# Kernel tuning notes

Measured on AMD Instinct MI355X. Metric: run time of the kernel, lower is better.

Reference implementation:

```python
import jax, jax.numpy as jnp
import numpy as np
import math

H, W = 1024, 1024

def setup_inputs() -> dict:
    key = jax.random.key(0)
    img = jax.random.uniform(key, (H, W), dtype=jnp.float32) * 255.0
    return {"InputImage": img}

def _phase_congruency(img):
    nrows, ncols = img.shape
    minWaveLength, mult = 3.0, 2.1
    nscale, norient = 5, 6
    sigmaOnf, k, cutOff, g = 0.55, 2.0, 0.5, 10.0
    eps = 1e-4

    cy, cx = nrows // 2, ncols // 2
    yy, xx = jnp.mgrid[0:nrows, 0:ncols]
    yy = (yy - cy) / nrows
    xx = (xx - cx) / ncols
    radius = jnp.sqrt(xx ** 2 + yy ** 2)
    radius = radius.at[cy, cx].set(1.0)
    theta = jnp.arctan2(-yy, xx)
    sintheta, costheta = jnp.sin(theta), jnp.cos(theta)

    # low-pass Butterworth (order 15, cutoff 0.45)
    normradius = radius / (jnp.abs(xx).max() * 2)
    lowpass = 1.0 / (1.0 + (normradius / 0.45) ** 30)

    # log-Gabor radial filters, [nscale, H, W]
    s = jnp.arange(nscale, dtype=jnp.float32)
    fo = 1.0 / (minWaveLength * mult ** s)            # [S]
    logGabor = jnp.exp(-jnp.log(radius[None] * (1.0 / fo)[:, None, None]) ** 2
                       / (2 * math.log(sigmaOnf) ** 2))
    annular = logGabor * lowpass[None]
    annular = annular.at[:, cy, cx].set(0.0)

    # angular spread, [norient, H, W]
    angl = jnp.arange(norient, dtype=jnp.float32) * (math.pi / norient)
    cosA, sinA = jnp.cos(angl), jnp.sin(angl)
    ds = sintheta[None] * cosA[:, None, None] - costheta[None] * sinA[:, None, None]
    dc = costheta[None] * cosA[:, None, None] + sintheta[None] * sinA[:, None, None]
    dtheta = jnp.minimum(jnp.abs(jnp.arctan2(ds, dc)) * (norient / 2), math.pi)
    spread = (jnp.cos(dtheta) + 1.0) / 2.0

    # full filter bank [O, S, H, W], shifted to DFT layout
    filt = jnp.fft.ifftshift(spread[:, None] * annular[None], axes=(-2, -1))

    F = jnp.fft.fft2(img)                              # complex64
    # cv2.idft is unscaled -> multiply numpy-style ifft by N
    z = jnp.fft.ifft2(filt * F[None, None]) * (nrows * ncols)   # [O,S,H,W]
    # original code: E (even) = channel 1 = Im(z), O (odd) = channel 0 = Re(z)
    E, O = z.imag, z.real
    An = jnp.abs(z)

    sumE = E.sum(axis=1)        # [O,H,W]
    sumO = O.sum(axis=1)
    sumAn = An.sum(axis=1)
    maxAn = An.max(axis=1)
    tau = jnp.median(An[:, 0].reshape(norient, -1), axis=1) / math.sqrt(math.log(4.0))

    XEnergy = jnp.sqrt(sumE ** 2 + sumO ** 2) + eps
    MeanE = sumE / XEnergy
    MeanO = sumO / XEnergy
    Energy = (E * MeanE[:, None] + O * MeanO[:, None]
              - jnp.abs(E * MeanO[:, None] - O * MeanE[:, None])).sum(axis=1)

    totalTau = tau * (1 - (1 / mult) ** nscale) / (1 - 1 / mult)   # [O]
    T = totalTau * math.sqrt(math.pi / 2) + k * totalTau * math.sqrt((4 - math.pi) / 2)
    Energy = jnp.maximum(Energy - T[:, None, None], 0.0)

    width = (sumAn / (maxAn + eps) - 1.0) / (nscale - 1)
    weight = 1.0 / (1.0 + jnp.exp((cutOff - width) * g))
    PC = weight * Energy / sumAn                       # [O,H,W]

    covx = PC * cosA[:, None, None]
    covy = PC * sinA[:, None, None]
    covx2 = (covx ** 2).sum(axis=0) / (norient / 2)
    covy2 = (covy ** 2).sum(axis=0) / (norient / 2)
    covxy = 4.0 * (covx * covy).sum(axis=0) / norient
    denom = jnp.sqrt(covxy ** 2 + (covx2 - covy2) ** 2) + eps
    M = (covy2 + covx2 + denom) / 2.0
    m = (covy2 + covx2 - denom) / 2.0
    return M, m

def reference(InputImage):
    M, m = _phase_congruency(InputImage)
    return (M, m)
```

## Files before the change

### kernel.cpp

```cpp
#include <hip/hip_runtime.h>
#include <math.h>

typedef float2 c2;

#define S_IDX(i) ((i) ^ (((i) >> 5) & 15))

__device__ __forceinline__ c2 cmul(c2 a, c2 b){
  return make_float2(a.x*b.x - a.y*b.y, a.x*b.y + a.y*b.x);
}

__constant__ float c_foinv[5] = {3.0f, 6.3f, 13.23f, 27.783f, 58.3443f};
__constant__ float c_lnfo[5]  = {1.0986123f, 1.8405496f, 2.5824700f, 3.3244106f, 4.0663219f};
__constant__ float c_angl[6]  = {0.0f, 0.5235988f, 1.0471976f, 1.5707963f, 2.0943951f, 2.6179939f};
__constant__ float c_cosA[6] = {1.0f, 0.8660254038f, 0.5f, 6.123233996e-17f, -0.5f, -0.8660254038f};
__constant__ float c_sinA[6] = {0.0f, 0.5f, 0.8660254038f, 1.0f, 0.8660254038f, 0.5f};

template<int SIGN>
__device__ __forceinline__ void make_tw(int t, c2* w){
#pragma unroll
  for (int k = 0; k < 5; ++k){
    const int s = 1 << (2*k);
    const float ang = (float)SIGN * 0.00613592315154256f * (float)(t & ~(s-1));
    sincosf(ang, &w[k].y, &w[k].x);
  }
}

template<int SIGN>
__device__ __forceinline__ void fft1024(c2* bufA, c2* bufB, int t, const c2* w){
  c2* cur = bufA; c2* oth = bufB;
#pragma unroll
  for (int k = 0; k < 5; ++k){
    const int s = 1 << (2*k);
    const int q = t & (s - 1);
    c2 a = cur[S_IDX(t)];
    c2 b = cur[S_IDX(t + 256)];
    c2 c = cur[S_IDX(t + 512)];
    c2 d = cur[S_IDX(t + 768)];
    c2 w1 = w[k];
    c2 w2 = cmul(w1, w1);
    c2 w3 = cmul(w2, w1);
    c2 apc = make_float2(a.x + c.x, a.y + c.y);
    c2 amc = make_float2(a.x - c.x, a.y - c.y);
    c2 bpd = make_float2(b.x + d.x, b.y + d.y);
    c2 bmd = make_float2(b.x - d.x, b.y - d.y);
    c2 y0 = make_float2(apc.x + bpd.x, apc.y + bpd.y);
    c2 e2 = make_float2(apc.x - bpd.x, apc.y - bpd.y);
    const float S4 = (float)SIGN;
    c2 u1 = make_float2(amc.x - S4*bmd.y, amc.y + S4*bmd.x);
    c2 u3 = make_float2(amc.x + S4*bmd.y, amc.y - S4*bmd.x);
    c2 y1 = cmul(u1, w1);
    c2 y2 = cmul(e2, w2);
    c2 y3 = cmul(u3, w3);
    const int bw = 4*t - 3*q;
    oth[S_IDX(bw)]       = y0;
    oth[S_IDX(bw + s)]   = y1;
    oth[S_IDX(bw + 2*s)] = y2;
    oth[S_IDX(bw + 3*s)] = y3;
    c2* tmp = cur; cur = oth; oth = tmp;
    __syncthreads();
  }
}

__device__ __forceinline__ float filt_eval(int q, int a, float xx,
                                           float cosA, float sinA, float foinv){
  const float yy = (float)(q < 512 ? q : q - 1024) * (1.0f/1024.0f);
  const float r2 = xx*xx + yy*yy;
  const bool isdc = (q == 0) && (a == 0);
  const float radius = isdc ? 1.0f : sqrtf(r2);
  const float tt = radius * (1.0f/0.45f);
  const float t2 = tt*tt, t4 = t2*t2, t8 = t4*t4, t16 = t8*t8;
  const float lp = 1.0f / (1.0f + t16*t8*t4*t2);
  const float lnr = logf(radius * foinv);
  const float lg = expf(-lnr*lnr * 1.3989572f);
  const float ir = 1.0f / radius;
  const float st = -yy * ir, ct = xx * ir;
  const float dsv = st*cosA - ct*sinA;
  const float dcv = ct*cosA + st*sinA;
  const float dth = fminf(fabsf(atan2f(dsv, dcv)) * 3.0f, 3.14159274f);
  const float spr = 0.5f * (cosf(dth) + 1.0f);
  const float f = lg * lp * spr;
  return isdc ? 0.0f : f;
}

__global__ __launch_bounds__(256) void k_filt_tab(float* __restrict__ lnrT, float* __restrict__ thetaT){
  const int a = blockIdx.x;
  const int t = threadIdx.x;
  const float xx = (float)(a < 512 ? a : a - 1024) * (1.0f/1024.0f);
#pragma unroll
  for (int j = 0; j < 4; ++j){
    const int q = t + 256*j;
    const float yy = (float)(q < 512 ? q : q - 1024) * (1.0f/1024.0f);
    const float radius = sqrtf(xx*xx + yy*yy);
    float lnr = logf(radius);
    if (a == 0 && q == 0) lnr = __int_as_float(0x7F800000);
    const float th = atan2f(-yy, xx);
    lnrT[a*1024 + q] = lnr;
    thetaT[a*1024 + q] = th;
  }
}

__global__ __launch_bounds__(256) void k_fft_fwd_real(const float* __restrict__ in, c2* __restrict__ out){
  const int t = threadIdx.x;
  __shared__ c2 bufA[1024];
  __shared__ c2 bufB[1024];
  c2 w[5]; make_tw<-1>(t, w);
  for (int rr = 0; rr < 4; ++rr){
    const int row = blockIdx.x * 4 + rr;
    const float* src = in + (size_t)row * 1024;
    c2* dst = out + (size_t)row * 1024;
#pragma unroll
    for (int j = 0; j < 4; ++j){
      const int q = t + 256*j;
      bufA[S_IDX(q)] = make_float2(src[q], 0.0f);
    }
    __syncthreads();
    fft1024<-1>(bufA, bufB, t, w);
#pragma unroll
    for (int j = 0; j < 4; ++j){ const int q = t + 256*j; dst[q] = bufB[S_IDX(q)]; }
    __syncthreads();
  }
}

__global__ __launch_bounds__(256) void k_fft_fwd_ip(c2* __restrict__ Z){
  const int t = threadIdx.x;
  c2* base = Z + (size_t)blockIdx.y * 1048576;
  __shared__ c2 bufA[1024];
  __shared__ c2 bufB[1024];
  c2 w[5]; make_tw<-1>(t, w);
  for (int rr = 0; rr < 4; ++rr){
    const int row = blockIdx.x * 4 + rr;
    c2* p = base + (size_t)row * 1024;
#pragma unroll
    for (int j = 0; j < 4; ++j){ const int q = t + 256*j; bufA[S_IDX(q)] = p[q]; }
    __syncthreads();
    fft1024<-1>(bufA, bufB, t, w);
#pragma unroll
    for (int j = 0; j < 4; ++j){ const int q = t + 256*j; p[q] = bufB[S_IDX(q)]; }
    __syncthreads();
  }
}

__global__ __launch_bounds__(256) void k_fft_inv_filter_t(const c2* __restrict__ F, c2* __restrict__ Z,
                                                          const float* __restrict__ lnrT,
                                                          const float* __restrict__ thetaT){
  const int t = threadIdx.x;
  const int gslot = blockIdx.y;
  const int orient = gslot / 5;
  const int scale = gslot - orient*5;
  const float lnfo = c_lnfo[scale];
  const float angl = c_angl[orient];
  __shared__ c2 bufA[1024];
  __shared__ c2 bufB[1024];
  c2 w[5]; make_tw<1>(t, w);
  for (int rr = 0; rr < 4; ++rr){
    const int row = blockIdx.x * 4 + rr;
    const c2* src = F + (size_t)row * 1024;
    const float* lnrR = lnrT + (size_t)row * 1024;
    const float* thR  = thetaT + (size_t)row * 1024;
    c2* dst = Z + (size_t)gslot * 1048576 + (size_t)row * 1024;
#pragma unroll
    for (int j = 0; j < 4; ++j){
      const int q = t + 256*j;
      const c2 v = src[q];
      const float lnr = lnrR[q];
      const float th  = thR[q];
      const float u = lnr + lnfo;
      const float lg = __expf(-u*u * 1.3989572f);
      const float lp = 1.0f / (1.0f + __expf(fmaf(30.0f, lnr, 23.955231f)));
      float d = th - angl;
      if (d <= -3.14159274f) d += 6.28318548f;
      const float dth = fminf(fabsf(d) * 3.0f, 3.14159274f);
      const float spr = 0.5f * (__cosf(dth) + 1.0f);
      const float f = lg * lp * spr;
      bufA[S_IDX(q)] = make_float2(v.x*f, v.y*f);
    }
    __syncthreads();
    fft1024<1>(bufA, bufB, t, w);
#pragma unroll
    for (int j = 0; j < 4; ++j){ const int q = t + 256*j; dst[q] = bufB[S_IDX(q)]; }
    __syncthreads();
  }
}

__global__ __launch_bounds__(256) void k_fft_inv_filter_b(const c2* __restrict__ F, c2* __restrict__ Z,
                                                          int slot0){
  const int t = threadIdx.x;
  const int gslot = slot0 + blockIdx.y;
  const int orient = gslot / 5;
  const int scale = gslot - orient*5;
  const float foinv = c_foinv[scale];
  const float cosA = c_cosA[orient], sinA = c_sinA[orient];
  __shared__ c2 bufA[1024];
  __shared__ c2 bufB[1024];
  c2 w[5]; make_tw<1>(t, w);
  for (int rr = 0; rr < 4; ++rr){
    const int row = blockIdx.x * 4 + rr;
    const c2* src = F + (size_t)row * 1024;
    c2* dst = Z + (size_t)blockIdx.y * 1048576 + (size_t)row * 1024;
    const float xx = (float)(row < 512 ? row : row - 1024) * (1.0f/1024.0f);
#pragma unroll
    for (int j = 0; j < 4; ++j){
      const int q = t + 256*j;
      const c2 v = src[q];
      const float f = filt_eval(q, row, xx, cosA, sinA, foinv);
      bufA[S_IDX(q)] = make_float2(v.x*f, v.y*f);
    }
    __syncthreads();
    fft1024<1>(bufA, bufB, t, w);
#pragma unroll
    for (int j = 0; j < 4; ++j){ const int q = t + 256*j; dst[q] = bufB[S_IDX(q)]; }
    __syncthreads();
  }
}

__global__ __launch_bounds__(256) void k_fft_inv_ip(c2* __restrict__ Z){
  const int t = threadIdx.x;
  c2* base = Z + (size_t)blockIdx.y * 1048576;
  __shared__ c2 bufA[1024];
  __shared__ c2 bufB[1024];
  c2 w[5]; make_tw<1>(t, w);
  for (int rr = 0; rr < 4; ++rr){
    const int row = blockIdx.x * 4 + rr;
    c2* p = base + (size_t)row * 1024;
#pragma unroll
    for (int j = 0; j < 4; ++j){ const int q = t + 256*j; bufA[S_IDX(q)] = p[q]; }
    __syncthreads();
    fft1024<1>(bufA, bufB, t, w);
#pragma unroll
    for (int j = 0; j < 4; ++j){ const int q = t + 256*j; p[q] = bufB[S_IDX(q)]; }
    __syncthreads();
  }
}

__global__ void k_transpose_ip(c2* __restrict__ Zb){
  __shared__ c2 A[32][33];
  __shared__ c2 B[32][33];
  c2* base = Zb + (size_t)blockIdx.y * 1048576;
  const int p = blockIdx.x;
  int i = (int)floorf((sqrtf(8.0f*(float)p + 1.0f) - 1.0f) * 0.5f);
  while ((i+1)*(i+2)/2 <= p) ++i;
  while (i*(i+1)/2 > p) --i;
  const int j = p - i*(i+1)/2;
  const int tx = threadIdx.x, ty = threadIdx.y;
  const int r0 = i*32, c0 = j*32;
#pragma unroll
  for (int jj = 0; jj < 32; jj += 8)
    A[ty+jj][tx] = base[(size_t)(r0+ty+jj)*1024 + c0+tx];
  if (i != j){
#pragma unroll
    for (int jj = 0; jj < 32; jj += 8)
      B[ty+jj][tx] = base[(size_t)(c0+ty+jj)*1024 + r0+tx];
  }
  __syncthreads();
#pragma unroll
  for (int jj = 0; jj < 32; jj += 8)
    base[(size_t)(c0+ty+jj)*1024 + r0+tx] = A[tx][ty+jj];
  if (i != j){
#pragma unroll
    for (int jj = 0; jj < 32; jj += 8)
      base[(size_t)(r0+ty+jj)*1024 + c0+tx] = B[tx][ty+jj];
  }
}


__device__ __forceinline__ unsigned amp_bits(const c2 v){
  return __float_as_uint(sqrtf(v.x*v.x + v.y*v.y));
}

__global__ __launch_bounds__(256) void k_med_p1b(const c2* __restrict__ Zb, size_t oStride,
                                                 unsigned* __restrict__ g1, int oBase){
  __shared__ unsigned h[4][4096];
  const int t = threadIdx.x;
  const int wv = t >> 6;
  const c2* z0 = Zb + (size_t)blockIdx.y * oStride;
  unsigned* gg = g1 + (size_t)(oBase + blockIdx.y) * 4096;
  for (int j = t; j < 4*4096; j += 256) ((unsigned*)h)[j] = 0;
  __syncthreads();
  const int base = blockIdx.x * 16384;
  for (int it = 0; it < 64; ++it){
    const unsigned bits = amp_bits(z0[base + it*256 + t]);
    atomicAdd(&h[wv][bits >> 20], 1u);
  }
  __syncthreads();
  for (int j = t; j < 4096; j += 256){
    const unsigned s = h[0][j] + h[1][j] + h[2][j] + h[3][j];
    if (s) atomicAdd(&gg[j], s);
  }
}

__global__ __launch_bounds__(256) void k_sel1b(const unsigned* __restrict__ g1,
                                               unsigned* __restrict__ sc1,
                                               unsigned* __restrict__ g2, int oBase){
  __shared__ unsigned partial[256];
  const int t = threadIdx.x;
  const int oo = oBase + blockIdx.x;
  const unsigned* gg = g1 + (size_t)oo * 4096;
  unsigned loc[16]; unsigned s = 0;
#pragma unroll
  for (int j = 0; j < 16; ++j){ loc[j] = gg[t*16 + j]; s += loc[j]; }
  partial[t] = s;
  __syncthreads();
  unsigned p = 0;
  for (int u = 0; u < t; ++u) p += partial[u];
  for (int which = 0; which < 2; ++which){
    const unsigned R = 524287u + (unsigned)which;
    if (R >= p && R - p < s){
      unsigned cum = p;
      for (int j = 0; j < 16; ++j){
        if (R - cum < loc[j]){ sc1[oo*4 + which*2] = (unsigned)(t*16 + j); sc1[oo*4 + which*2+1] = R - cum; break; }
        cum += loc[j];
      }
    }
  }
  for (int j = t; j < 8192; j += 256) g2[(size_t)oo*8192 + j] = 0;
}

__global__ __launch_bounds__(256) void k_med_p2b(const c2* __restrict__ Zb, size_t oStride,
                                                 const unsigned* __restrict__ sc1,
                                                 unsigned* __restrict__ g2, int oBase){
  __shared__ unsigned h[2][4096];
  const int t = threadIdx.x;
  const int oo = oBase + blockIdx.y;
  const c2* z0 = Zb + (size_t)blockIdx.y * oStride;
  unsigned* gg = g2 + (size_t)oo * 8192;
  for (int j = t; j < 8192; j += 256) ((unsigned*)h)[j] = 0;
  __syncthreads();
  const unsigned b0 = sc1[oo*4 + 0], b1 = sc1[oo*4 + 2];
  const int base = blockIdx.x * 16384;
  for (int it = 0; it < 64; ++it){
    const unsigned bits = amp_bits(z0[base + it*256 + t]);
    const unsigned top = bits >> 20;
    const unsigned mid = (bits >> 8) & 4095u;
    if (top == b0)      atomicAdd(&h[0][mid], 1u);
    else if (top == b1) atomicAdd(&h[1][mid], 1u);
  }
  __syncthreads();
  for (int j = t; j < 4096; j += 256){
    if (h[0][j]) atomicAdd(&gg[j], h[0][j]);
    if (h[1][j]) atomicAdd(&gg[4096 + j], h[1][j]);
  }
}

__global__ __launch_bounds__(256) void k_sel2b(const unsigned* __restrict__ g2,
                                               const unsigned* __restrict__ sc1,
                                               unsigned* __restrict__ sc2,
                                               unsigned* __restrict__ g3, int oBase){
  __shared__ unsigned partial[256];
  const int t = threadIdx.x;
  const int oo = oBase + blockIdx.x;
  const unsigned b0 = sc1[oo*4+0], lr0 = sc1[oo*4+1], b1 = sc1[oo*4+2], lr1 = sc1[oo*4+3];
  for (int which = 0; which < 2; ++which){
    const unsigned* hh = g2 + (size_t)oo*8192 + ((which == 1 && b1 != b0) ? 4096 : 0);
    const unsigned R = which ? lr1 : lr0;
    unsigned loc[16]; unsigned s = 0;
#pragma unroll
    for (int j = 0; j < 16; ++j){ loc[j] = hh[t*16 + j]; s += loc[j]; }
    partial[t] = s;
    __syncthreads();
    unsigned p = 0;
    for (int u = 0; u < t; ++u) p += partial[u];
    if (R >= p && R - p < s){
      unsigned cum = p;
      for (int j = 0; j < 16; ++j){
        if (R - cum < loc[j]){ sc2[oo*4 + which*2] = (unsigned)(t*16 + j); sc2[oo*4 + which*2+1] = R - cum; break; }
        cum += loc[j];
      }
    }
    __syncthreads();
  }
  for (int j = t; j < 512; j += 256) g3[(size_t)oo*512 + j] = 0;
}

__global__ __launch_bounds__(256) void k_med_p3b(const c2* __restrict__ Zb, size_t oStride,
                                                 const unsigned* __restrict__ sc1,
                                                 const unsigned* __restrict__ sc2,
                                                 unsigned* __restrict__ g3, int oBase){
  __shared__ unsigned h[2][256];
  const int t = threadIdx.x;
  const int oo = oBase + blockIdx.y;
  const c2* z0 = Zb + (size_t)blockIdx.y * oStride;
  unsigned* gg = g3 + (size_t)oo * 512;
  h[0][t] = 0; h[1][t] = 0;
  __syncthreads();
  const unsigned k0 = (sc1[oo*4+0] << 12) | sc2[oo*4+0];
  const unsigned k1 = (sc1[oo*4+2] << 12) | sc2[oo*4+2];
  const int base = blockIdx.x * 16384;
  for (int it = 0; it < 64; ++it){
    const unsigned bits = amp_bits(z0[base + it*256 + t]);
    const unsigned key = bits >> 8;
    if (key == k0)       atomicAdd(&h[0][bits & 255u], 1u);
    else if (key == k1)  atomicAdd(&h[1][bits & 255u], 1u);
  }
  __syncthreads();
  if (h[0][t]) atomicAdd(&gg[t], h[0][t]);
  if (h[1][t]) atomicAdd(&gg[256 + t], h[1][t]);
}

__global__ __launch_bounds__(256) void k_sel3b(const unsigned* __restrict__ g3,
                                               const unsigned* __restrict__ sc1,
                                               const unsigned* __restrict__ sc2,
                                               float* __restrict__ Tval, int oBase){
  __shared__ unsigned partial[256];
  __shared__ float vres[2];
  const int t = threadIdx.x;
  const int oo = oBase + blockIdx.x;
  const unsigned k0 = (sc1[oo*4+0] << 12) | sc2[oo*4+0];
  const unsigned k1 = (sc1[oo*4+2] << 12) | sc2[oo*4+2];
  for (int which = 0; which < 2; ++which){
    const unsigned* hh = g3 + (size_t)oo*512 + ((which == 1 && k1 != k0) ? 256 : 0);
    const unsigned R = which ? sc2[oo*4+3] : sc2[oo*4+1];
    partial[t] = hh[t];
    __syncthreads();
    unsigned p = 0;
    for (int u = 0; u < t; ++u) p += partial[u];
    if (R >= p && R - p < partial[t]){
      const unsigned key = which ? k1 : k0;
      vres[which] = __uint_as_float((key << 8) | (unsigned)t);
    }
    __syncthreads();
  }
  if (t == 0){
    const float med = 0.5f * (vres[0] + vres[1]);
    const float tau = med / 1.17741001f;
    const float totalTau = tau * 1.8623464f;
    const float T = totalTau * 1.25331414f + 2.0f * totalTau * 0.65513638f;
    Tval[oo] = T;
  }
}


__global__ __launch_bounds__(256) void k_pix_all(const c2* __restrict__ Z, const float* __restrict__ Tval,
                                                 float* __restrict__ out){
  const int i = blockIdx.x * 256 + threadIdx.x;
  float covx2 = 0.f, covy2 = 0.f, covxy = 0.f;
#pragma unroll
  for (int o = 0; o < 6; ++o){
    const float T = Tval[o];
    float E[5], O[5];
    float sumE = 0.f, sumO = 0.f, sumAn = 0.f, maxAn = 0.f;
#pragma unroll
    for (int s = 0; s < 5; ++s){
      const c2 z = Z[(size_t)(o*5 + s) * 1048576 + i];
      O[s] = z.x; E[s] = z.y;
      const float an = sqrtf(z.x*z.x + z.y*z.y);
      sumE += E[s]; sumO += O[s]; sumAn += an; maxAn = fmaxf(maxAn, an);
    }
    const float XE = sqrtf(sumE*sumE + sumO*sumO) + 1e-4f;
    const float ME = sumE / XE, MO = sumO / XE;
    float energy = 0.f;
#pragma unroll
    for (int s = 0; s < 5; ++s)
      energy += E[s]*ME + O[s]*MO - fabsf(E[s]*MO - O[s]*ME);
    energy = fmaxf(energy - T, 0.f);
    const float width = (sumAn / (maxAn + 1e-4f) - 1.0f) * 0.25f;
    const float weight = 1.0f / (1.0f + expf((0.5f - width) * 10.0f));
    const float PC = weight * energy / sumAn;
    const float cx = PC * c_cosA[o], cy = PC * c_sinA[o];
    covx2 += cx*cx; covy2 += cy*cy; covxy += cx*cy;
  }
  covx2 *= (1.0f/3.0f);
  covy2 *= (1.0f/3.0f);
  covxy *= (4.0f/6.0f);
  const float dnm = sqrtf(covxy*covxy + (covx2 - covy2)*(covx2 - covy2)) + 1e-4f;
  const float ss = covy2 + covx2;
  out[i] = (ss + dnm) / 2.0f;
  out[1048576 + i] = (ss - dnm) / 2.0f;
}


__global__ __launch_bounds__(256) void k_pix(const c2* __restrict__ Z, const float* __restrict__ Tp,
                                             float cA, float sA,
                                             float* __restrict__ ax2, float* __restrict__ ay2,
                                             float* __restrict__ axy, int first){
  const int i = blockIdx.x * 256 + threadIdx.x;
  const float T = *Tp;
  float E[5], O[5];
  float sumE = 0.f, sumO = 0.f, sumAn = 0.f, maxAn = 0.f;
#pragma unroll
  for (int s = 0; s < 5; ++s){
    const c2 z = Z[(size_t)s * 1048576 + i];
    O[s] = z.x; E[s] = z.y;
    const float an = sqrtf(z.x*z.x + z.y*z.y);
    sumE += E[s]; sumO += O[s]; sumAn += an; maxAn = fmaxf(maxAn, an);
  }
  const float XE = sqrtf(sumE*sumE + sumO*sumO) + 1e-4f;
  const float ME = sumE / XE, MO = sumO / XE;
  float energy = 0.f;
#pragma unroll
  for (int s = 0; s < 5; ++s)
    energy += E[s]*ME + O[s]*MO - fabsf(E[s]*MO - O[s]*ME);
  energy = fmaxf(energy - T, 0.f);
  const float width = (sumAn / (maxAn + 1e-4f) - 1.0f) * 0.25f;
  const float weight = 1.0f / (1.0f + expf((0.5f - width) * 10.0f));
  const float PC = weight * energy / sumAn;
  const float cx = PC * cA, cy = PC * sA;
  if (first){ ax2[i] = cx*cx; ay2[i] = cy*cy; axy[i] = cx*cy; }
  else      { ax2[i] += cx*cx; ay2[i] += cy*cy; axy[i] += cx*cy; }
}

__global__ __launch_bounds__(256) void k_final(const float* __restrict__ ax2, const float* __restrict__ ay2,
                                               const float* __restrict__ axy, float* __restrict__ out){
  const int i = blockIdx.x * 256 + threadIdx.x;
  const float cx2 = ax2[i] / 3.0f;
  const float cy2 = ay2[i] / 3.0f;
  const float cxy = 4.0f * axy[i] / 6.0f;
  const float dnm = sqrtf(cxy*cxy + (cx2 - cy2)*(cx2 - cy2)) + 1e-4f;
  const float ss = cy2 + cx2;
  out[i] = (ss + dnm) / 2.0f;
  out[1048576 + i] = (ss - dnm) / 2.0f;
}

extern "C" void kernel_launch(void* const* d_in, const int* in_sizes, int n_in,
                              void* d_out, int out_size, void* d_ws, size_t ws_size,
                              hipStream_t stream){
  (void)in_sizes; (void)n_in; (void)out_size;
  const float* img = (const float*)d_in[0];
  float* out = (float*)d_out;
  char* w = (char*)d_ws;

  const dim3 th(256);
  const dim3 thT(32, 8);

  if (ws_size >= (size_t)268435456){
    c2* F  = (c2*)(w);
    c2* Z  = (c2*)(w + 8388608);
    float* lnrT   = (float*)(w + 260046848);
    float* thetaT = (float*)(w + 264241152);
    unsigned* g1  = (unsigned*)(w);
    unsigned* g2  = (unsigned*)(w + 98304);
    unsigned* g3  = (unsigned*)(w + 294912);
    unsigned* sc1 = (unsigned*)(w + 307200);
    unsigned* sc2 = (unsigned*)(w + 307328);
    float* Tval   = (float*)(w + 307456);

    k_filt_tab<<<dim3(1024), th, 0, stream>>>(lnrT, thetaT);

    k_fft_fwd_real<<<dim3(256), th, 0, stream>>>(img, F);
    k_transpose_ip<<<dim3(528, 1), thT, 0, stream>>>(F);
    k_fft_fwd_ip<<<dim3(256, 1), th, 0, stream>>>(F);

    k_fft_inv_filter_t<<<dim3(256, 30), th, 0, stream>>>(F, Z, lnrT, thetaT);
    k_transpose_ip<<<dim3(528, 30), thT, 0, stream>>>(Z);
    k_fft_inv_ip<<<dim3(256, 30), th, 0, stream>>>(Z);

    hipMemsetAsync(g1, 0, 6*16384, stream);
    const size_t oStride = (size_t)5 * 1048576;
    k_med_p1b<<<dim3(64, 6), th, 0, stream>>>(Z, oStride, g1, 0);
    k_sel1b<<<dim3(6), th, 0, stream>>>(g1, sc1, g2, 0);
    k_med_p2b<<<dim3(64, 6), th, 0, stream>>>(Z, oStride, sc1, g2, 0);
    k_sel2b<<<dim3(6), th, 0, stream>>>(g2, sc1, sc2, g3, 0);
    k_med_p3b<<<dim3(64, 6), th, 0, stream>>>(Z, oStride, sc1, sc2, g3, 0);
    k_sel3b<<<dim3(6), th, 0, stream>>>(g3, sc1, sc2, Tval, 0);

    k_pix_all<<<dim3(4096), th, 0, stream>>>(Z, Tval, out);
  } else {
    c2* F   = (c2*)(w);
    c2* C5  = (c2*)(w + 8388608);
    float* ax2 = (float*)(w + 50331648);
    float* ay2 = ax2 + 1048576;
    float* axy = ay2 + 1048576;
    unsigned* g1  = (unsigned*)(w + 62914560);
    unsigned* g2  = (unsigned*)(w + 62930944);
    unsigned* g3  = (unsigned*)(w + 62963712);
    unsigned* sc1 = (unsigned*)(w + 62965760);
    unsigned* sc2 = (unsigned*)(w + 62965888);
    float* Tval   = (float*)(w + 62966016);

    k_fft_fwd_real<<<dim3(256), th, 0, stream>>>(img, F);
    k_transpose_ip<<<dim3(528, 1), thT, 0, stream>>>(F);
    k_fft_fwd_ip<<<dim3(256, 1), th, 0, stream>>>(F);

    for (int o = 0; o < 6; ++o){
      k_fft_inv_filter_b<<<dim3(256, 5), th, 0, stream>>>(F, C5, o*5);
      k_transpose_ip<<<dim3(528, 5), thT, 0, stream>>>(C5);
      k_fft_inv_ip<<<dim3(256, 5), th, 0, stream>>>(C5);

      hipMemsetAsync(g1, 0, 16384, stream);
      k_med_p1b<<<dim3(64, 1), th, 0, stream>>>(C5, 0, g1, 0);
      k_sel1b<<<dim3(1), th, 0, stream>>>(g1, sc1, g2, 0);
      k_med_p2b<<<dim3(64, 1), th, 0, stream>>>(C5, 0, sc1, g2, 0);
      k_sel2b<<<dim3(1), th, 0, stream>>>(g2, sc1, sc2, g3, 0);
      k_med_p3b<<<dim3(64, 1), th, 0, stream>>>(C5, 0, sc1, sc2, g3, 0);
      k_sel3b<<<dim3(1), th, 0, stream>>>(g3, sc1, sc2, Tval, 0);

      const double a = (double)o * (M_PI/6.0);
      k_pix<<<dim3(4096), th, 0, stream>>>(C5, Tval, (float)cos(a), (float)sin(a),
                                           ax2, ay2, axy, (o == 0) ? 1 : 0);
    }
    k_final<<<dim3(4096), th, 0, stream>>>(ax2, ay2, axy, out);
  }
}
```

Measured before the change: 420.9 us.

## Replace transpose plus row FFT with column-slab FFT in shared memory

The in-place global transpose kernel followed by a row FFT pass is replaced by one kernel that loads an 8-column slab of 1024 rows into LDS, runs the 1024-point FFT on each column there, and writes it back in place. This removes a full read/write sweep of the 30-channel complex buffer and a kernel launch per stage. The filter coordinate convention is flipped (row→yy, column→xx) so the spectrum stays in natural rather than transposed layout. The trade-off is about 74KB of LDS per block, which lowers occupancy, and column loads of only 8 consecutive complex values per row (64-byte segments), so global access is less coalesced.

```diff
diff --git a/kernel.cpp b/kernel.cpp
--- a/kernel.cpp
+++ b/kernel.cpp
@@ -4,6 +4,7 @@
 typedef float2 c2;
 
 #define S_IDX(i) ((i) ^ (((i) >> 5) & 15))
+#define SLAB_STRIDE 1025
 
 __device__ __forceinline__ c2 cmul(c2 a, c2 b){
   return make_float2(a.x*b.x - a.y*b.y, a.x*b.y + a.y*b.x);
@@ -61,12 +62,11 @@
   }
 }
 
-__device__ __forceinline__ float filt_eval(int q, int a, float xx,
+__device__ __forceinline__ float filt_eval(int c, int r, float yy,
                                            float cosA, float sinA, float foinv){
-  const float yy = (float)(q < 512 ? q : q - 1024) * (1.0f/1024.0f);
-  const float r2 = xx*xx + yy*yy;
-  const bool isdc = (q == 0) && (a == 0);
-  const float radius = isdc ? 1.0f : sqrtf(r2);
+  const float xx = (float)(c < 512 ? c : c - 1024) * (1.0f/1024.0f);
+  const bool isdc = (c == 0) && (r == 0);
+  const float radius = isdc ? 1.0f : sqrtf(xx*xx + yy*yy);
   const float tt = radius * (1.0f/0.45f);
   const float t2 = tt*tt, t4 = t2*t2, t8 = t4*t4, t16 = t8*t8;
   const float lp = 1.0f / (1.0f + t16*t8*t4*t2);
@@ -83,19 +83,18 @@
 }
 
 __global__ __launch_bounds__(256) void k_filt_tab(float* __restrict__ lnrT, float* __restrict__ thetaT){
-  const int a = blockIdx.x;
-  const int t = threadIdx.x;
-  const float xx = (float)(a < 512 ? a : a - 1024) * (1.0f/1024.0f);
+  const int r = blockIdx.x;
+  const int t = threadIdx.x;
+  const float yy = (float)(r < 512 ? r : r - 1024) * (1.0f/1024.0f);
 #pragma unroll
   for (int j = 0; j < 4; ++j){
-    const int q = t + 256*j;
-    const float yy = (float)(q < 512 ? q : q - 1024) * (1.0f/1024.0f);
+    const int c = t + 256*j;
+    const float xx = (float)(c < 512 ? c : c - 1024) * (1.0f/1024.0f);
     const float radius = sqrtf(xx*xx + yy*yy);
     float lnr = logf(radius);
-    if (a == 0 && q == 0) lnr = __int_as_float(0x7F800000);
-    const float th = atan2f(-yy, xx);
-    lnrT[a*1024 + q] = lnr;
-    thetaT[a*1024 + q] = th;
+    if (r == 0 && c == 0) lnr = __int_as_float(0x7F800000);
+    lnrT[r*1024 + c] = lnr;
+    thetaT[r*1024 + c] = atan2f(-yy, xx);
   }
 }
 
@@ -121,22 +120,31 @@
   }
 }
 
-__global__ __launch_bounds__(256) void k_fft_fwd_ip(c2* __restrict__ Z){
-  const int t = threadIdx.x;
+template<int SIGN>
+__global__ __launch_bounds__(256) void k_fft_col_slab(c2* __restrict__ Z){
+  __shared__ c2 slab[8 * SLAB_STRIDE];
+  __shared__ c2 bufB[1024];
   c2* base = Z + (size_t)blockIdx.y * 1048576;
-  __shared__ c2 bufA[1024];
-  __shared__ c2 bufB[1024];
-  c2 w[5]; make_tw<-1>(t, w);
-  for (int rr = 0; rr < 4; ++rr){
-    const int row = blockIdx.x * 4 + rr;
-    c2* p = base + (size_t)row * 1024;
-#pragma unroll
-    for (int j = 0; j < 4; ++j){ const int q = t + 256*j; bufA[S_IDX(q)] = p[q]; }
-    __syncthreads();
-    fft1024<-1>(bufA, bufB, t, w);
-#pragma unroll
-    for (int j = 0; j < 4; ++j){ const int q = t + 256*j; p[q] = bufB[S_IDX(q)]; }
-    __syncthreads();
+  const int t = threadIdx.x;
+  const int col0 = blockIdx.x * 8;
+  const int cl = t & 7;
+  const int rw = t >> 3;
+  c2 w[5]; make_tw<SIGN>(t, w);
+  for (int ch = 0; ch < 32; ++ch){
+    const int row = ch * 32 + rw;
+    slab[cl * SLAB_STRIDE + S_IDX(row)] = base[(size_t)row * 1024 + col0 + cl];
+  }
+  __syncthreads();
+  for (int c = 0; c < 8; ++c){
+    c2* colp = slab + c * SLAB_STRIDE;
+#pragma unroll
+    for (int j = 0; j < 4; ++j) bufB[t + 256*j] = colp[t + 256*j];
+    __syncthreads();
+    fft1024<SIGN>(bufB, colp, t, w);
+  }
+  for (int ch = 0; ch < 32; ++ch){
+    const int row = ch * 32 + rw;
+    base[(size_t)row * 1024 + col0 + cl] = slab[cl * SLAB_STRIDE + S_IDX(row)];
   }
 }
 
@@ -197,12 +205,12 @@
     const int row = blockIdx.x * 4 + rr;
     const c2* src = F + (size_t)row * 1024;
     c2* dst = Z + (size_t)blockIdx.y * 1048576 + (size_t)row * 1024;
-    const float xx = (float)(row < 512 ? row : row - 1024) * (1.0f/1024.0f);
+    const float yy = (float)(row < 512 ? row : row - 1024) * (1.0f/1024.0f);
 #pragma unroll
     for (int j = 0; j < 4; ++j){
       const int q = t + 256*j;
       const c2 v = src[q];
-      const float f = filt_eval(q, row, xx, cosA, sinA, foinv);
+      const float f = filt_eval(q, row, yy, cosA, sinA, foinv);
       bufA[S_IDX(q)] = make_float2(v.x*f, v.y*f);
     }
     __syncthreads();
@@ -210,55 +218,6 @@
 #pragma unroll
     for (int j = 0; j < 4; ++j){ const int q = t + 256*j; dst[q] = bufB[S_IDX(q)]; }
     __syncthreads();
-  }
-}
-
-__global__ __launch_bounds__(256) void k_fft_inv_ip(c2* __restrict__ Z){
-  const int t = threadIdx.x;
-  c2* base = Z + (size_t)blockIdx.y * 1048576;
-  __shared__ c2 bufA[1024];
-  __shared__ c2 bufB[1024];
-  c2 w[5]; make_tw<1>(t, w);
-  for (int rr = 0; rr < 4; ++rr){
-    const int row = blockIdx.x * 4 + rr;
-    c2* p = base + (size_t)row * 1024;
-#pragma unroll
-    for (int j = 0; j < 4; ++j){ const int q = t + 256*j; bufA[S_IDX(q)] = p[q]; }
-    __syncthreads();
-    fft1024<1>(bufA, bufB, t, w);
-#pragma unroll
-    for (int j = 0; j < 4; ++j){ const int q = t + 256*j; p[q] = bufB[S_IDX(q)]; }
-    __syncthreads();
-  }
-}
-
-__global__ void k_transpose_ip(c2* __restrict__ Zb){
-  __shared__ c2 A[32][33];
-  __shared__ c2 B[32][33];
-  c2* base = Zb + (size_t)blockIdx.y * 1048576;
-  const int p = blockIdx.x;
-  int i = (int)floorf((sqrtf(8.0f*(float)p + 1.0f) - 1.0f) * 0.5f);
-  while ((i+1)*(i+2)/2 <= p) ++i;
-  while (i*(i+1)/2 > p) --i;
-  const int j = p - i*(i+1)/2;
-  const int tx = threadIdx.x, ty = threadIdx.y;
-  const int r0 = i*32, c0 = j*32;
-#pragma unroll
-  for (int jj = 0; jj < 32; jj += 8)
-    A[ty+jj][tx] = base[(size_t)(r0+ty+jj)*1024 + c0+tx];
-  if (i != j){
-#pragma unroll
-    for (int jj = 0; jj < 32; jj += 8)
-      B[ty+jj][tx] = base[(size_t)(c0+ty+jj)*1024 + r0+tx];
-  }
-  __syncthreads();
-#pragma unroll
-  for (int jj = 0; jj < 32; jj += 8)
-    base[(size_t)(c0+ty+jj)*1024 + r0+tx] = A[tx][ty+jj];
-  if (i != j){
-#pragma unroll
-    for (int jj = 0; jj < 32; jj += 8)
-      base[(size_t)(r0+ty+jj)*1024 + c0+tx] = B[tx][ty+jj];
   }
 }
 
@@ -519,7 +478,6 @@
   char* w = (char*)d_ws;
 
   const dim3 th(256);
-  const dim3 thT(32, 8);
 
   if (ws_size >= (size_t)268435456){
     c2* F  = (c2*)(w);
@@ -536,12 +494,10 @@
     k_filt_tab<<<dim3(1024), th, 0, stream>>>(lnrT, thetaT);
 
     k_fft_fwd_real<<<dim3(256), th, 0, stream>>>(img, F);
-    k_transpose_ip<<<dim3(528, 1), thT, 0, stream>>>(F);
-    k_fft_fwd_ip<<<dim3(256, 1), th, 0, stream>>>(F);
+    k_fft_col_slab<-1><<<dim3(128, 1), th, 0, stream>>>(F);
 
     k_fft_inv_filter_t<<<dim3(256, 30), th, 0, stream>>>(F, Z, lnrT, thetaT);
-    k_transpose_ip<<<dim3(528, 30), thT, 0, stream>>>(Z);
-    k_fft_inv_ip<<<dim3(256, 30), th, 0, stream>>>(Z);
+    k_fft_col_slab<1><<<dim3(128, 30), th, 0, stream>>>(Z);
 
     hipMemsetAsync(g1, 0, 6*16384, stream);
     const size_t oStride = (size_t)5 * 1048576;
@@ -567,13 +523,11 @@
     float* Tval   = (float*)(w + 62966016);
 
     k_fft_fwd_real<<<dim3(256), th, 0, stream>>>(img, F);
-    k_transpose_ip<<<dim3(528, 1), thT, 0, stream>>>(F);
-    k_fft_fwd_ip<<<dim3(256, 1), th, 0, stream>>>(F);
+    k_fft_col_slab<-1><<<dim3(128, 1), th, 0, stream>>>(F);
 
     for (int o = 0; o < 6; ++o){
       k_fft_inv_filter_b<<<dim3(256, 5), th, 0, stream>>>(F, C5, o*5);
-      k_transpose_ip<<<dim3(528, 5), thT, 0, stream>>>(C5);
-      k_fft_inv_ip<<<dim3(256, 5), th, 0, stream>>>(C5);
+      k_fft_col_slab<1><<<dim3(128, 5), th, 0, stream>>>(C5);
 
       hipMemsetAsync(g1, 0, 16384, stream);
       k_med_p1b<<<dim3(64, 1), th, 0, stream>>>(C5, 0, g1, 0);
```

Result: no change. 422.9 us (+0.5%).
